# Optimization experiments

Measured on AMD Instinct MI355X. Metric: run time of the kernel, lower is better.

## Reference

```python
import jax, jax.numpy as jnp
import numpy as np

DIM = 2048
RATE = 4
LAYER_ID = 0
DYNAMIC_SCALE = 0.01
EPS = 1e-5


def setup_inputs() -> dict:
    key = jax.random.key(0)
    k1, k2, k3, k4 = jax.random.split(key, 4)
    b, l = 2, 4096
    h = jax.random.normal(k1, (b, l, RATE, DIM), dtype=jnp.float32)
    h_o = jax.random.normal(k2, (b, l, DIM), dtype=jnp.float32)
    # LayerNorm affine params
    ln_gamma = jnp.ones((DIM,), dtype=jnp.float32)
    ln_beta = jnp.zeros((DIM,), dtype=jnp.float32)
    # dynamic fns: init to zeros in module; use small random so math is nontrivial
    dynamic_alpha_fn = 0.02 * jax.random.normal(k3, (DIM, RATE + 1), dtype=jnp.float32)
    dynamic_beta_fn = 0.02 * jax.random.normal(k4, (DIM,), dtype=jnp.float32)
    # static alpha: [init_alpha0 | eye(rate)] -> (rate, rate+1)
    init_alpha0 = np.zeros((RATE, 1), dtype=np.float32)
    init_alpha0[LAYER_ID % RATE, 0] = 1.0
    static_alpha = jnp.asarray(np.concatenate([init_alpha0, np.eye(RATE, dtype=np.float32)], axis=1))
    static_beta = jnp.ones((RATE,), dtype=jnp.float32)
    return {
        "h": h,
        "h_o": h_o,
        "ln_gamma": ln_gamma,
        "ln_beta": ln_beta,
        "dynamic_alpha_fn": dynamic_alpha_fn,
        "dynamic_beta_fn": dynamic_beta_fn,
        "static_alpha": static_alpha,
        "static_beta": static_beta,
    }


def _layernorm(x, gamma, beta):
    mu = jnp.mean(x, axis=-1, keepdims=True)
    var = jnp.mean(jnp.square(x - mu), axis=-1, keepdims=True)
    return (x - mu) * jax.lax.rsqrt(var + EPS) * gamma + beta


def reference(h, h_o, ln_gamma, ln_beta, dynamic_alpha_fn, dynamic_beta_fn, static_alpha, static_beta):
    # h: (b, l, n=rate, d); h_o: (b, l, d)
    norm_h = _layernorm(h, ln_gamma, ln_beta)
    # dynamic alpha: (b,l,n,rate+1)
    dyn_alpha = jnp.einsum("blnd,dk->blnk", norm_h, dynamic_alpha_fn) * DYNAMIC_SCALE
    alpha = dyn_alpha + static_alpha[None, None, :, :]  # (b,l,n,k)
    # mix: alpha^T @ h over n -> (b,l,k,d)
    mix_h = jnp.einsum("blnk,blnd->blkd", alpha, h)
    # dynamic beta: (b,l,n)
    dyn_beta = jnp.einsum("blnd,d->bln", norm_h, dynamic_beta_fn) * DYNAMIC_SCALE
    beta = dyn_beta + static_beta[None, None, :]  # (b,l,rate)
    # depth connection: broadcast residual-branch output over rate streams
    out = h_o[:, :, None, :] * beta[..., None] + mix_h[..., 1:, :]
    return out
```

## Files before the change

kernel.cpp:

```cpp
#include <hip/hip_runtime.h>


#define NDIM   2048
#define NRATE  4
#define DSCALE 0.01f
#define LEPS   1e-5f

typedef float vfloat4 __attribute__((ext_vector_type(4)));

#define WS_PK2 16
#define WS_PK4 4112

template <int C>
__device__ __forceinline__ float dppmv(float x) {
    return __builtin_bit_cast(float,
        __builtin_amdgcn_update_dpp(0, __builtin_bit_cast(int, x), C, 0xF, 0xF, true));
}

__device__ __forceinline__ float wsum(float x) {
    x += dppmv<0x111>(x);
    x += dppmv<0x112>(x);
    x += dppmv<0x114>(x);
    x += dppmv<0x118>(x);
    x += dppmv<0x142>(x);
    x += dppmv<0x143>(x);
    return x;
}

__global__ __launch_bounds__(256) void hc_prep(
    const float* __restrict__ g_, const float* __restrict__ b_,
    const float* __restrict__ Afn, const float* __restrict__ Bfn,
    float* __restrict__ ws)
{
    __shared__ float s_red[4][10];
    const int t = threadIdx.x;
    const int lane = t & 63, wave = t >> 6;
    float acc[10];
    #pragma unroll
    for (int v = 0; v < 10; v++) acc[v] = 0.f;
    #pragma unroll
    for (int i = 0; i < 8; i++) {
        const int d = t * 8 + i;
        const float g  = g_[d];
        const float b  = b_[d];
        const float db = Bfn[d];
        const float a1 = Afn[d*5+1], a2 = Afn[d*5+2], a3 = Afn[d*5+3], a4 = Afn[d*5+4];
        *(float2*)(ws + WS_PK2 + 2*d) = make_float2(g, db);
        *(float4*)(ws + WS_PK4 + 4*d) = make_float4(a1, a2, a3, a4);
        acc[0] = fmaf(g, a1, acc[0]); acc[1] = fmaf(g, a2, acc[1]);
        acc[2] = fmaf(g, a3, acc[2]); acc[3] = fmaf(g, a4, acc[3]);
        acc[4] = fmaf(b, a1, acc[4]); acc[5] = fmaf(b, a2, acc[5]);
        acc[6] = fmaf(b, a3, acc[6]); acc[7] = fmaf(b, a4, acc[7]);
        acc[8] = fmaf(g, db, acc[8]); acc[9] = fmaf(b, db, acc[9]);
    }
    #pragma unroll
    for (int v = 0; v < 10; v++) {
        float w = wsum(acc[v]);
        if (lane == 63) s_red[wave][v] = w;
    }
    __syncthreads();
    if (t < 10) ws[t] = s_red[0][t] + s_red[1][t] + s_red[2][t] + s_red[3][t];
}

__global__ __launch_bounds__(256) void hc_main(
    const float* __restrict__ h,
    const float* __restrict__ h_o,
    const float* __restrict__ sA,
    const float* __restrict__ sB,
    const float* __restrict__ ws,
    float* __restrict__ out)
{
    __shared__ float s_red[4][28];
    __shared__ float s_bc[28];

    const int t    = threadIdx.x;
    const int lane = t & 63;
    const int wave = t >> 6;
    const size_t pbase = (size_t)blockIdx.x * (NRATE * NDIM);
    const int dc0 = 4 * t;
    const int dc1 = 1024 + 4 * t;

    float hv[NRATE][8];
    #pragma unroll
    for (int n = 0; n < NRATE; n++) {
        const float4 r0 = *(const float4*)(h + pbase + n * NDIM + dc0);
        const float4 r1 = *(const float4*)(h + pbase + n * NDIM + dc1);
        hv[n][0] = r0.x; hv[n][1] = r0.y; hv[n][2] = r0.z; hv[n][3] = r0.w;
        hv[n][4] = r1.x; hv[n][5] = r1.y; hv[n][6] = r1.z; hv[n][7] = r1.w;
    }
    const float4 ro0 = *(const float4*)(h_o + (size_t)blockIdx.x * NDIM + dc0);
    const float4 ro1 = *(const float4*)(h_o + (size_t)blockIdx.x * NDIM + dc1);

    const float GA0 = ws[0], GA1 = ws[1], GA2 = ws[2], GA3 = ws[3];
    const float BA0 = ws[4], BA1 = ws[5], BA2 = ws[6], BA3 = ws[7];
    const float GB  = ws[8], BB  = ws[9];

    float S[NRATE]  = {0.f, 0.f, 0.f, 0.f};
    float SS[NRATE] = {0.f, 0.f, 0.f, 0.f};
    float Q[NRATE]  = {0.f, 0.f, 0.f, 0.f};
    float Pk[NRATE][4] = {};
    #pragma unroll
    for (int c = 0; c < 2; c++) {
        const int dc = c ? dc1 : dc0;
        #pragma unroll
        for (int i = 0; i < 4; i++) {
            const int d = dc + i;
            const float2 gb = *(const float2*)(ws + WS_PK2 + 2 * d);
            const float4 a  = *(const float4*)(ws + WS_PK4 + 4 * d);
            #pragma unroll
            for (int n = 0; n < NRATE; n++) {
                const float x = hv[n][c * 4 + i];
                S[n] += x;
                SS[n] = fmaf(x, x, SS[n]);
                const float xg = x * gb.x;
                Pk[n][0] = fmaf(xg, a.x, Pk[n][0]);
                Pk[n][1] = fmaf(xg, a.y, Pk[n][1]);
                Pk[n][2] = fmaf(xg, a.z, Pk[n][2]);
                Pk[n][3] = fmaf(xg, a.w, Pk[n][3]);
                Q[n]     = fmaf(xg, gb.y, Q[n]);
            }
        }
    }

    float red[28];
    #pragma unroll
    for (int n = 0; n < NRATE; n++) {
        red[n]     = S[n];
        red[4 + n] = SS[n];
        red[8 + n] = Q[n];
        #pragma unroll
        for (int k = 0; k < 4; k++) red[12 + n * 4 + k] = Pk[n][k];
    }
    #pragma unroll
    for (int v = 0; v < 28; v++) {
        float w = wsum(red[v]);
        if (lane == 63) s_red[wave][v] = w;
    }
    __syncthreads();
    if (t < 28) s_bc[t] = s_red[0][t] + s_red[1][t] + s_red[2][t] + s_red[3][t];
    __syncthreads();

    float alpha_f[NRATE][4], beta_f[NRATE];
    #pragma unroll
    for (int n = 0; n < NRATE; n++) {
        const float m   = s_bc[n] * (1.0f / NDIM);
        const float var = s_bc[4 + n] * (1.0f / NDIM) - m * m;
        const float rs  = rsqrtf(var + LEPS);
        const float p0 = s_bc[12 + n * 4 + 0], p1 = s_bc[12 + n * 4 + 1];
        const float p2 = s_bc[12 + n * 4 + 2], p3 = s_bc[12 + n * 4 + 3];
        alpha_f[n][0] = fmaf(DSCALE, fmaf(rs, fmaf(-m, GA0, p0), BA0), sA[n * 5 + 1]);
        alpha_f[n][1] = fmaf(DSCALE, fmaf(rs, fmaf(-m, GA1, p1), BA1), sA[n * 5 + 2]);
        alpha_f[n][2] = fmaf(DSCALE, fmaf(rs, fmaf(-m, GA2, p2), BA2), sA[n * 5 + 3]);
        alpha_f[n][3] = fmaf(DSCALE, fmaf(rs, fmaf(-m, GA3, p3), BA3), sA[n * 5 + 4]);
        beta_f[n]     = fmaf(DSCALE, fmaf(rs, fmaf(-m, GB, s_bc[8 + n]), BB), sB[n]);
    }

    float ho[8];
    ho[0] = ro0.x; ho[1] = ro0.y; ho[2] = ro0.z; ho[3] = ro0.w;
    ho[4] = ro1.x; ho[5] = ro1.y; ho[6] = ro1.z; ho[7] = ro1.w;

    #pragma unroll
    for (int j = 0; j < NRATE; j++) {
        float o[8];
        #pragma unroll
        for (int i = 0; i < 8; i++) {
            float acc = ho[i] * beta_f[j];
            #pragma unroll
            for (int n = 0; n < NRATE; n++) acc = fmaf(alpha_f[n][j], hv[n][i], acc);
            o[i] = acc;
        }
        vfloat4 w0 = { o[0], o[1], o[2], o[3] };
        vfloat4 w1 = { o[4], o[5], o[6], o[7] };
        __builtin_nontemporal_store(w0, (vfloat4*)(out + pbase + j * NDIM + dc0));
        __builtin_nontemporal_store(w1, (vfloat4*)(out + pbase + j * NDIM + dc1));
    }
}

extern "C" void kernel_launch(void* const* d_in, const int* in_sizes, int n_in,
                              void* d_out, int out_size, void* d_ws, size_t ws_size,
                              hipStream_t stream) {
    const float* h   = (const float*)d_in[0];
    const float* h_o = (const float*)d_in[1];
    const float* g   = (const float*)d_in[2];
    const float* b   = (const float*)d_in[3];
    const float* A   = (const float*)d_in[4];
    const float* Bf  = (const float*)d_in[5];
    const float* sA  = (const float*)d_in[6];
    const float* sB  = (const float*)d_in[7];
    float* out = (float*)d_out;
    float* ws  = (float*)d_ws;

    const int P = in_sizes[1] / NDIM;
    hc_prep<<<1, 256, 0, stream>>>(g, b, A, Bf, ws);
    hc_main<<<P, 256, 0, stream>>>(h, h_o, sA, sB, ws, out);
}
```

Baseline: 490.2 us.

## Process four positions per block with register prefetch of next row

Each block now handles four consecutive positions instead of one. The per-dimension gamma/beta/alpha weights are loaded into registers once and reused across all four. The next position's h row is prefetched into registers while the current one is reduced and written, so load latency overlaps compute. Launch bounds are set to 3 blocks per CU to cap register use. The trade-offs are higher register pressure, a four-fold smaller grid, and an assumption that P is divisible by four.

```diff
diff --git a/kernel.cpp b/kernel.cpp
--- a/kernel.cpp
+++ b/kernel.cpp
@@ -3,6 +3,7 @@
 
 #define NDIM   2048
 #define NRATE  4
+#define POSN   4
 #define DSCALE 0.01f
 #define LEPS   1e-5f
 
@@ -62,7 +63,7 @@
     if (t < 10) ws[t] = s_red[0][t] + s_red[1][t] + s_red[2][t] + s_red[3][t];
 }
 
-__global__ __launch_bounds__(256) void hc_main(
+__global__ __launch_bounds__(256, 3) void hc_main(
     const float* __restrict__ h,
     const float* __restrict__ h_o,
     const float* __restrict__ sA,
@@ -76,103 +77,142 @@
     const int t    = threadIdx.x;
     const int lane = t & 63;
     const int wave = t >> 6;
-    const size_t pbase = (size_t)blockIdx.x * (NRATE * NDIM);
     const int dc0 = 4 * t;
     const int dc1 = 1024 + 4 * t;
-
-    float hv[NRATE][8];
-    #pragma unroll
-    for (int n = 0; n < NRATE; n++) {
-        const float4 r0 = *(const float4*)(h + pbase + n * NDIM + dc0);
-        const float4 r1 = *(const float4*)(h + pbase + n * NDIM + dc1);
-        hv[n][0] = r0.x; hv[n][1] = r0.y; hv[n][2] = r0.z; hv[n][3] = r0.w;
-        hv[n][4] = r1.x; hv[n][5] = r1.y; hv[n][6] = r1.z; hv[n][7] = r1.w;
-    }
-    const float4 ro0 = *(const float4*)(h_o + (size_t)blockIdx.x * NDIM + dc0);
-    const float4 ro1 = *(const float4*)(h_o + (size_t)blockIdx.x * NDIM + dc1);
 
     const float GA0 = ws[0], GA1 = ws[1], GA2 = ws[2], GA3 = ws[3];
     const float BA0 = ws[4], BA1 = ws[5], BA2 = ws[6], BA3 = ws[7];
     const float GB  = ws[8], BB  = ws[9];
 
-    float S[NRATE]  = {0.f, 0.f, 0.f, 0.f};
-    float SS[NRATE] = {0.f, 0.f, 0.f, 0.f};
-    float Q[NRATE]  = {0.f, 0.f, 0.f, 0.f};
-    float Pk[NRATE][4] = {};
+    float2 gbr[8];
+    float4 ar[8];
     #pragma unroll
     for (int c = 0; c < 2; c++) {
         const int dc = c ? dc1 : dc0;
         #pragma unroll
         for (int i = 0; i < 4; i++) {
-            const int d = dc + i;
-            const float2 gb = *(const float2*)(ws + WS_PK2 + 2 * d);
-            const float4 a  = *(const float4*)(ws + WS_PK4 + 4 * d);
+            gbr[c * 4 + i] = *(const float2*)(ws + WS_PK2 + 2 * (dc + i));
+            ar[c * 4 + i]  = *(const float4*)(ws + WS_PK4 + 4 * (dc + i));
+        }
+    }
+
+    const size_t p0 = (size_t)blockIdx.x * POSN;
+
+    float hvC[NRATE][8];
+    {
+        const size_t pbase = p0 * (size_t)(NRATE * NDIM);
+        #pragma unroll
+        for (int n = 0; n < NRATE; n++) {
+            const float4 r0 = *(const float4*)(h + pbase + n * NDIM + dc0);
+            const float4 r1 = *(const float4*)(h + pbase + n * NDIM + dc1);
+            hvC[n][0] = r0.x; hvC[n][1] = r0.y; hvC[n][2] = r0.z; hvC[n][3] = r0.w;
+            hvC[n][4] = r1.x; hvC[n][5] = r1.y; hvC[n][6] = r1.z; hvC[n][7] = r1.w;
+        }
+    }
+
+    #pragma unroll
+    for (int it = 0; it < POSN; ++it) {
+        const size_t pos   = p0 + it;
+        const size_t pbase = pos * (size_t)(NRATE * NDIM);
+
+        const float4 ro0 = *(const float4*)(h_o + pos * NDIM + dc0);
+        const float4 ro1 = *(const float4*)(h_o + pos * NDIM + dc1);
+        float hvN[NRATE][8];
+        if (it + 1 < POSN) {
+            const size_t nbase = pbase + (size_t)(NRATE * NDIM);
             #pragma unroll
             for (int n = 0; n < NRATE; n++) {
-                const float x = hv[n][c * 4 + i];
-                S[n] += x;
-                SS[n] = fmaf(x, x, SS[n]);
-                const float xg = x * gb.x;
-                Pk[n][0] = fmaf(xg, a.x, Pk[n][0]);
-                Pk[n][1] = fmaf(xg, a.y, Pk[n][1]);
-                Pk[n][2] = fmaf(xg, a.z, Pk[n][2]);
-                Pk[n][3] = fmaf(xg, a.w, Pk[n][3]);
-                Q[n]     = fmaf(xg, gb.y, Q[n]);
+                const float4 r0 = *(const float4*)(h + nbase + n * NDIM + dc0);
+                const float4 r1 = *(const float4*)(h + nbase + n * NDIM + dc1);
+                hvN[n][0] = r0.x; hvN[n][1] = r0.y; hvN[n][2] = r0.z; hvN[n][3] = r0.w;
+                hvN[n][4] = r1.x; hvN[n][5] = r1.y; hvN[n][6] = r1.z; hvN[n][7] = r1.w;
             }
         }
-    }
-
-    float red[28];
-    #pragma unroll
-    for (int n = 0; n < NRATE; n++) {
-        red[n]     = S[n];
-        red[4 + n] = SS[n];
-        red[8 + n] = Q[n];
-        #pragma unroll
-        for (int k = 0; k < 4; k++) red[12 + n * 4 + k] = Pk[n][k];
-    }
-    #pragma unroll
-    for (int v = 0; v < 28; v++) {
-        float w = wsum(red[v]);
-        if (lane == 63) s_red[wave][v] = w;
-    }
-    __syncthreads();
-    if (t < 28) s_bc[t] = s_red[0][t] + s_red[1][t] + s_red[2][t] + s_red[3][t];
-    __syncthreads();
-
-    float alpha_f[NRATE][4], beta_f[NRATE];
-    #pragma unroll
-    for (int n = 0; n < NRATE; n++) {
-        const float m   = s_bc[n] * (1.0f / NDIM);
-        const float var = s_bc[4 + n] * (1.0f / NDIM) - m * m;
-        const float rs  = rsqrtf(var + LEPS);
-        const float p0 = s_bc[12 + n * 4 + 0], p1 = s_bc[12 + n * 4 + 1];
-        const float p2 = s_bc[12 + n * 4 + 2], p3 = s_bc[12 + n * 4 + 3];
-        alpha_f[n][0] = fmaf(DSCALE, fmaf(rs, fmaf(-m, GA0, p0), BA0), sA[n * 5 + 1]);
-        alpha_f[n][1] = fmaf(DSCALE, fmaf(rs, fmaf(-m, GA1, p1), BA1), sA[n * 5 + 2]);
-        alpha_f[n][2] = fmaf(DSCALE, fmaf(rs, fmaf(-m, GA2, p2), BA2), sA[n * 5 + 3]);
-        alpha_f[n][3] = fmaf(DSCALE, fmaf(rs, fmaf(-m, GA3, p3), BA3), sA[n * 5 + 4]);
-        beta_f[n]     = fmaf(DSCALE, fmaf(rs, fmaf(-m, GB, s_bc[8 + n]), BB), sB[n]);
-    }
-
-    float ho[8];
-    ho[0] = ro0.x; ho[1] = ro0.y; ho[2] = ro0.z; ho[3] = ro0.w;
-    ho[4] = ro1.x; ho[5] = ro1.y; ho[6] = ro1.z; ho[7] = ro1.w;
-
-    #pragma unroll
-    for (int j = 0; j < NRATE; j++) {
-        float o[8];
-        #pragma unroll
-        for (int i = 0; i < 8; i++) {
-            float acc = ho[i] * beta_f[j];
-            #pragma unroll
-            for (int n = 0; n < NRATE; n++) acc = fmaf(alpha_f[n][j], hv[n][i], acc);
-            o[i] = acc;
-        }
-        vfloat4 w0 = { o[0], o[1], o[2], o[3] };
-        vfloat4 w1 = { o[4], o[5], o[6], o[7] };
-        __builtin_nontemporal_store(w0, (vfloat4*)(out + pbase + j * NDIM + dc0));
-        __builtin_nontemporal_store(w1, (vfloat4*)(out + pbase + j * NDIM + dc1));
+
+        float S[NRATE]  = {0.f, 0.f, 0.f, 0.f};
+        float SS[NRATE] = {0.f, 0.f, 0.f, 0.f};
+        float Q[NRATE]  = {0.f, 0.f, 0.f, 0.f};
+        float Pk[NRATE][4] = {};
+        #pragma unroll
+        for (int c = 0; c < 2; c++) {
+            #pragma unroll
+            for (int i = 0; i < 4; i++) {
+                const float2 gb = gbr[c * 4 + i];
+                const float4 a  = ar[c * 4 + i];
+                #pragma unroll
+                for (int n = 0; n < NRATE; n++) {
+                    const float x = hvC[n][c * 4 + i];
+                    S[n] += x;
+                    SS[n] = fmaf(x, x, SS[n]);
+                    const float xg = x * gb.x;
+                    Pk[n][0] = fmaf(xg, a.x, Pk[n][0]);
+                    Pk[n][1] = fmaf(xg, a.y, Pk[n][1]);
+                    Pk[n][2] = fmaf(xg, a.z, Pk[n][2]);
+                    Pk[n][3] = fmaf(xg, a.w, Pk[n][3]);
+                    Q[n]     = fmaf(xg, gb.y, Q[n]);
+                }
+            }
+        }
+
+        float red[28];
+        #pragma unroll
+        for (int n = 0; n < NRATE; n++) {
+            red[n]     = S[n];
+            red[4 + n] = SS[n];
+            red[8 + n] = Q[n];
+            #pragma unroll
+            for (int k = 0; k < 4; k++) red[12 + n * 4 + k] = Pk[n][k];
+        }
+        #pragma unroll
+        for (int v = 0; v < 28; v++) {
+            float w = wsum(red[v]);
+            if (lane == 63) s_red[wave][v] = w;
+        }
+        __syncthreads();
+        if (t < 28) s_bc[t] = s_red[0][t] + s_red[1][t] + s_red[2][t] + s_red[3][t];
+        __syncthreads();
+
+        float alpha_f[NRATE][4], beta_f[NRATE];
+        #pragma unroll
+        for (int n = 0; n < NRATE; n++) {
+            const float m   = s_bc[n] * (1.0f / NDIM);
+            const float var = s_bc[4 + n] * (1.0f / NDIM) - m * m;
+            const float rs  = rsqrtf(var + LEPS);
+            const float pk0 = s_bc[12 + n * 4 + 0], pk1 = s_bc[12 + n * 4 + 1];
+            const float pk2 = s_bc[12 + n * 4 + 2], pk3 = s_bc[12 + n * 4 + 3];
+            alpha_f[n][0] = fmaf(DSCALE, fmaf(rs, fmaf(-m, GA0, pk0), BA0), sA[n * 5 + 1]);
+            alpha_f[n][1] = fmaf(DSCALE, fmaf(rs, fmaf(-m, GA1, pk1), BA1), sA[n * 5 + 2]);
+            alpha_f[n][2] = fmaf(DSCALE, fmaf(rs, fmaf(-m, GA2, pk2), BA2), sA[n * 5 + 3]);
+            alpha_f[n][3] = fmaf(DSCALE, fmaf(rs, fmaf(-m, GA3, pk3), BA3), sA[n * 5 + 4]);
+            beta_f[n]     = fmaf(DSCALE, fmaf(rs, fmaf(-m, GB, s_bc[8 + n]), BB), sB[n]);
+        }
+
+        float ho[8];
+        ho[0] = ro0.x; ho[1] = ro0.y; ho[2] = ro0.z; ho[3] = ro0.w;
+        ho[4] = ro1.x; ho[5] = ro1.y; ho[6] = ro1.z; ho[7] = ro1.w;
+
+        #pragma unroll
+        for (int j = 0; j < NRATE; j++) {
+            float o[8];
+            #pragma unroll
+            for (int i = 0; i < 8; i++) {
+                float acc = ho[i] * beta_f[j];
+                #pragma unroll
+                for (int n = 0; n < NRATE; n++) acc = fmaf(alpha_f[n][j], hvC[n][i], acc);
+                o[i] = acc;
+            }
+            vfloat4 w0 = { o[0], o[1], o[2], o[3] };
+            vfloat4 w1 = { o[4], o[5], o[6], o[7] };
+            __builtin_nontemporal_store(w0, (vfloat4*)(out + pbase + j * NDIM + dc0));
+            __builtin_nontemporal_store(w1, (vfloat4*)(out + pbase + j * NDIM + dc1));
+        }
+
+        if (it + 1 < POSN) {
+            #pragma unroll
+            for (int n = 0; n < NRATE; n++)
+                #pragma unroll
+                for (int i = 0; i < 8; i++) hvC[n][i] = hvN[n][i];
+        }
     }
 }
 
@@ -192,5 +232,5 @@
 
     const int P = in_sizes[1] / NDIM;
     hc_prep<<<1, 256, 0, stream>>>(g, b, A, Bf, ws);
-    hc_main<<<P, 256, 0, stream>>>(h, h_o, sA, sB, ws, out);
-}
+    hc_main<<<P / POSN, 256, 0, stream>>>(h, h_o, sA, sB, ws, out);
+}
```

Measured after the change: 507.4 us. 3.5% more time.

## Map one wavefront per position and re-read h in a second pass

Applied to the files above, without the earlier changes.

Each 64-lane wavefront now handles a whole position instead of a 256-thread block sharing one. This removes the LDS reduction and both block barriers, using a DPP reduction followed by a readlane broadcast. h is no longer kept in registers: it is streamed once for the statistics and read again for the output pass, trading extra global/L2 traffic for lower register pressure and no block sync. gamma and beta_fn are read directly from the inputs instead of a packed workspace.

```diff
diff --git a/kernel.cpp b/kernel.cpp
--- a/kernel.cpp
+++ b/kernel.cpp
@@ -8,8 +8,7 @@
 
 typedef float vfloat4 __attribute__((ext_vector_type(4)));
 
-#define WS_PK2 16
-#define WS_PK4 4112
+#define WS_PK4 16
 
 template <int C>
 __device__ __forceinline__ float dppmv(float x) {
@@ -25,6 +24,11 @@
     x += dppmv<0x142>(x);
     x += dppmv<0x143>(x);
     return x;
+}
+
+__device__ __forceinline__ float bcast63(float x) {
+    return __builtin_bit_cast(float,
+        __builtin_amdgcn_readlane(__builtin_bit_cast(int, x), 63));
 }
 
 __global__ __launch_bounds__(256) void hc_prep(
@@ -45,7 +49,6 @@
         const float b  = b_[d];
         const float db = Bfn[d];
         const float a1 = Afn[d*5+1], a2 = Afn[d*5+2], a3 = Afn[d*5+3], a4 = Afn[d*5+4];
-        *(float2*)(ws + WS_PK2 + 2*d) = make_float2(g, db);
         *(float4*)(ws + WS_PK4 + 4*d) = make_float4(a1, a2, a3, a4);
         acc[0] = fmaf(g, a1, acc[0]); acc[1] = fmaf(g, a2, acc[1]);
         acc[2] = fmaf(g, a3, acc[2]); acc[3] = fmaf(g, a4, acc[3]);
@@ -65,31 +68,18 @@
 __global__ __launch_bounds__(256) void hc_main(
     const float* __restrict__ h,
     const float* __restrict__ h_o,
+    const float* __restrict__ g_,
+    const float* __restrict__ Bfn,
     const float* __restrict__ sA,
     const float* __restrict__ sB,
     const float* __restrict__ ws,
     float* __restrict__ out)
 {
-    __shared__ float s_red[4][28];
-    __shared__ float s_bc[28];
-
-    const int t    = threadIdx.x;
-    const int lane = t & 63;
-    const int wave = t >> 6;
-    const size_t pbase = (size_t)blockIdx.x * (NRATE * NDIM);
-    const int dc0 = 4 * t;
-    const int dc1 = 1024 + 4 * t;
-
-    float hv[NRATE][8];
-    #pragma unroll
-    for (int n = 0; n < NRATE; n++) {
-        const float4 r0 = *(const float4*)(h + pbase + n * NDIM + dc0);
-        const float4 r1 = *(const float4*)(h + pbase + n * NDIM + dc1);
-        hv[n][0] = r0.x; hv[n][1] = r0.y; hv[n][2] = r0.z; hv[n][3] = r0.w;
-        hv[n][4] = r1.x; hv[n][5] = r1.y; hv[n][6] = r1.z; hv[n][7] = r1.w;
-    }
-    const float4 ro0 = *(const float4*)(h_o + (size_t)blockIdx.x * NDIM + dc0);
-    const float4 ro1 = *(const float4*)(h_o + (size_t)blockIdx.x * NDIM + dc1);
+    const int lane = threadIdx.x & 63;
+    const int wv   = threadIdx.x >> 6;
+    const size_t pos   = (size_t)blockIdx.x * 4 + wv;
+    const size_t pbase = pos * (size_t)(NRATE * NDIM);
+    const int d0 = lane * 4;
 
     const float GA0 = ws[0], GA1 = ws[1], GA2 = ws[2], GA3 = ws[3];
     const float BA0 = ws[4], BA1 = ws[5], BA2 = ws[6], BA3 = ws[7];
@@ -99,25 +89,31 @@
     float SS[NRATE] = {0.f, 0.f, 0.f, 0.f};
     float Q[NRATE]  = {0.f, 0.f, 0.f, 0.f};
     float Pk[NRATE][4] = {};
-    #pragma unroll
-    for (int c = 0; c < 2; c++) {
-        const int dc = c ? dc1 : dc0;
+    #pragma unroll 4
+    for (int c = 0; c < 8; ++c) {
+        const int d = d0 + 256 * c;
+        const float4 g4 = *(const float4*)(g_ + d);
+        const float4 q4 = *(const float4*)(Bfn + d);
+        float4 a4[4];
         #pragma unroll
-        for (int i = 0; i < 4; i++) {
-            const int d = dc + i;
-            const float2 gb = *(const float2*)(ws + WS_PK2 + 2 * d);
-            const float4 a  = *(const float4*)(ws + WS_PK4 + 4 * d);
+        for (int i = 0; i < 4; ++i) a4[i] = *(const float4*)(ws + WS_PK4 + 4 * (d + i));
+        const float gs[4] = {g4.x, g4.y, g4.z, g4.w};
+        const float qs[4] = {q4.x, q4.y, q4.z, q4.w};
+        #pragma unroll
+        for (int n = 0; n < NRATE; ++n) {
+            const float4 x4 = *(const float4*)(h + pbase + n * NDIM + d);
+            const float xs[4] = {x4.x, x4.y, x4.z, x4.w};
             #pragma unroll
-            for (int n = 0; n < NRATE; n++) {
-                const float x = hv[n][c * 4 + i];
+            for (int i = 0; i < 4; ++i) {
+                const float x = xs[i];
                 S[n] += x;
                 SS[n] = fmaf(x, x, SS[n]);
-                const float xg = x * gb.x;
-                Pk[n][0] = fmaf(xg, a.x, Pk[n][0]);
-                Pk[n][1] = fmaf(xg, a.y, Pk[n][1]);
-                Pk[n][2] = fmaf(xg, a.z, Pk[n][2]);
-                Pk[n][3] = fmaf(xg, a.w, Pk[n][3]);
-                Q[n]     = fmaf(xg, gb.y, Q[n]);
+                const float xg = x * gs[i];
+                Pk[n][0] = fmaf(xg, a4[i].x, Pk[n][0]);
+                Pk[n][1] = fmaf(xg, a4[i].y, Pk[n][1]);
+                Pk[n][2] = fmaf(xg, a4[i].z, Pk[n][2]);
+                Pk[n][3] = fmaf(xg, a4[i].w, Pk[n][3]);
+                Q[n]     = fmaf(xg, qs[i], Q[n]);
             }
         }
     }
@@ -131,48 +127,53 @@
         #pragma unroll
         for (int k = 0; k < 4; k++) red[12 + n * 4 + k] = Pk[n][k];
     }
+    float sums[28];
     #pragma unroll
-    for (int v = 0; v < 28; v++) {
-        float w = wsum(red[v]);
-        if (lane == 63) s_red[wave][v] = w;
-    }
-    __syncthreads();
-    if (t < 28) s_bc[t] = s_red[0][t] + s_red[1][t] + s_red[2][t] + s_red[3][t];
-    __syncthreads();
+    for (int v = 0; v < 28; v++) sums[v] = bcast63(wsum(red[v]));
 
     float alpha_f[NRATE][4], beta_f[NRATE];
     #pragma unroll
     for (int n = 0; n < NRATE; n++) {
-        const float m   = s_bc[n] * (1.0f / NDIM);
-        const float var = s_bc[4 + n] * (1.0f / NDIM) - m * m;
+        const float m   = sums[n] * (1.0f / NDIM);
+        const float var = sums[4 + n] * (1.0f / NDIM) - m * m;
         const float rs  = rsqrtf(var + LEPS);
-        const float p0 = s_bc[12 + n * 4 + 0], p1 = s_bc[12 + n * 4 + 1];
-        const float p2 = s_bc[12 + n * 4 + 2], p3 = s_bc[12 + n * 4 + 3];
-        alpha_f[n][0] = fmaf(DSCALE, fmaf(rs, fmaf(-m, GA0, p0), BA0), sA[n * 5 + 1]);
-        alpha_f[n][1] = fmaf(DSCALE, fmaf(rs, fmaf(-m, GA1, p1), BA1), sA[n * 5 + 2]);
-        alpha_f[n][2] = fmaf(DSCALE, fmaf(rs, fmaf(-m, GA2, p2), BA2), sA[n * 5 + 3]);
-        alpha_f[n][3] = fmaf(DSCALE, fmaf(rs, fmaf(-m, GA3, p3), BA3), sA[n * 5 + 4]);
-        beta_f[n]     = fmaf(DSCALE, fmaf(rs, fmaf(-m, GB, s_bc[8 + n]), BB), sB[n]);
+        const float pk0 = sums[12 + n * 4 + 0], pk1 = sums[12 + n * 4 + 1];
+        const float pk2 = sums[12 + n * 4 + 2], pk3 = sums[12 + n * 4 + 3];
+        alpha_f[n][0] = fmaf(DSCALE, fmaf(rs, fmaf(-m, GA0, pk0), BA0), sA[n * 5 + 1]);
+        alpha_f[n][1] = fmaf(DSCALE, fmaf(rs, fmaf(-m, GA1, pk1), BA1), sA[n * 5 + 2]);
+        alpha_f[n][2] = fmaf(DSCALE, fmaf(rs, fmaf(-m, GA2, pk2), BA2), sA[n * 5 + 3]);
+        alpha_f[n][3] = fmaf(DSCALE, fmaf(rs, fmaf(-m, GA3, pk3), BA3), sA[n * 5 + 4]);
+        beta_f[n]     = fmaf(DSCALE, fmaf(rs, fmaf(-m, GB, sums[8 + n]), BB), sB[n]);
     }
 
-    float ho[8];
-    ho[0] = ro0.x; ho[1] = ro0.y; ho[2] = ro0.z; ho[3] = ro0.w;
-    ho[4] = ro1.x; ho[5] = ro1.y; ho[6] = ro1.z; ho[7] = ro1.w;
-
-    #pragma unroll
-    for (int j = 0; j < NRATE; j++) {
-        float o[8];
+    const float* hp  = h + pbase;
+    const float* hop = h_o + pos * NDIM;
+    float* op = out + pbase;
+    #pragma unroll 4
+    for (int c = 0; c < 8; ++c) {
+        const int d = d0 + 256 * c;
+        const float4 x0 = *(const float4*)(hp + 0 * NDIM + d);
+        const float4 x1 = *(const float4*)(hp + 1 * NDIM + d);
+        const float4 x2 = *(const float4*)(hp + 2 * NDIM + d);
+        const float4 x3 = *(const float4*)(hp + 3 * NDIM + d);
+        const float4 ho = *(const float4*)(hop + d);
+        const float hs[4] = {ho.x, ho.y, ho.z, ho.w};
+        const float xa[4][4] = {{x0.x, x0.y, x0.z, x0.w},
+                                {x1.x, x1.y, x1.z, x1.w},
+                                {x2.x, x2.y, x2.z, x2.w},
+                                {x3.x, x3.y, x3.z, x3.w}};
         #pragma unroll
-        for (int i = 0; i < 8; i++) {
-            float acc = ho[i] * beta_f[j];
+        for (int j = 0; j < NRATE; ++j) {
+            vfloat4 o;
             #pragma unroll
-            for (int n = 0; n < NRATE; n++) acc = fmaf(alpha_f[n][j], hv[n][i], acc);
-            o[i] = acc;
+            for (int i = 0; i < 4; ++i) {
+                float acc = hs[i] * beta_f[j];
+                #pragma unroll
+                for (int n = 0; n < NRATE; ++n) acc = fmaf(alpha_f[n][j], xa[n][i], acc);
+                o[i] = acc;
+            }
+            __builtin_nontemporal_store(o, (vfloat4*)(op + j * NDIM + d));
         }
-        vfloat4 w0 = { o[0], o[1], o[2], o[3] };
-        vfloat4 w1 = { o[4], o[5], o[6], o[7] };
-        __builtin_nontemporal_store(w0, (vfloat4*)(out + pbase + j * NDIM + dc0));
-        __builtin_nontemporal_store(w1, (vfloat4*)(out + pbase + j * NDIM + dc1));
     }
 }
 
@@ -192,5 +193,5 @@
 
     const int P = in_sizes[1] / NDIM;
     hc_prep<<<1, 256, 0, stream>>>(g, b, A, Bf, ws);
-    hc_main<<<P, 256, 0, stream>>>(h, h_o, sA, sB, ws, out);
+    hc_main<<<P / 4, 256, 0, stream>>>(h, h_o, g, Bf, sA, sB, ws, out);
 }
```

Measured after the change: 508.6 us. +3.7%, slower.
